# Optimization experiments

Hardware: AMD Instinct MI355X
Metric: run time of the kernel (lower is better)

Reference implementation:

```python
import jax, jax.numpy as jnp
import numpy as np
from jax import lax

EPS = 1e-10

def _ln(x, g, b):
    m = x.mean(-1, keepdims=True)
    v = x.var(-1, keepdims=True)
    return (x - m) / jnp.sqrt(v + 1e-5) * g + b

def _gather(t, idx):
    # t: (B, HW, c), idx: (B, HW, d) -> (B, HW, d, c); out[n,i,k,:] = t[n, idx[n,i,k], :]
    return jax.vmap(lambda tn, In: tn[In])(t, idx)

def setup_inputs() -> dict:
    key = jax.random.key(0)
    ks = jax.random.split(key, 20)
    b, v, c, d, h, w, hid, ksz = 2, 2, 128, 64, 64, 64, 256, 5
    hw = h * w
    Bf = b * v  # v_1 == 1 target view per reference view
    std = 0.02
    return {
        'features_mv': jax.random.normal(ks[0], (b, v, c, h, w), jnp.float32),
        'warp_indices': jax.random.randint(ks[1], (Bf, hw, d), 0, hw, jnp.int32),
        'depth_prob': jax.random.uniform(ks[2], (Bf, hw, d), jnp.float32),
        'ln1_g': jnp.ones((c,), jnp.float32), 'ln1_b': jnp.zeros((c,), jnp.float32),
        'wq': jax.random.normal(ks[3], (c, c), jnp.float32) * std, 'bq': jnp.zeros((c,), jnp.float32),
        'wk': jax.random.normal(ks[4], (c, c), jnp.float32) * std, 'bk': jnp.zeros((c,), jnp.float32),
        'wv': jax.random.normal(ks[5], (c, c), jnp.float32) * std, 'bv': jnp.zeros((c,), jnp.float32),
        'k_pe': jax.random.normal(ks[6], (1, 1, d), jnp.float32) * std,
        'v_pe': jax.random.normal(ks[7], (1, 1, d), jnp.float32) * std,
        'rpe': jax.random.normal(ks[8], (1, 1, d), jnp.float32) * std,
        'proj_w': jax.random.normal(ks[9], (c, c), jnp.float32) * std, 'proj_b': jnp.zeros((c,), jnp.float32),
        'ln2_g': jnp.ones((c,), jnp.float32), 'ln2_b': jnp.zeros((c,), jnp.float32),
        'fc1_w': jax.random.normal(ks[10], (c, hid), jnp.float32) * std, 'fc1_b': jnp.zeros((hid,), jnp.float32),
        'dw_w': jax.random.normal(ks[11], (hid, 1, ksz, ksz), jnp.float32) * std, 'dw_b': jnp.zeros((hid,), jnp.float32),
        'fc2_w': jax.random.normal(ks[12], (hid, c), jnp.float32) * std, 'fc2_b': jnp.zeros((c,), jnp.float32),
    }

def reference(features_mv, warp_indices, depth_prob, ln1_g, ln1_b, wq, bq, wk, bk, wv, bv,
              k_pe, v_pe, rpe, proj_w, proj_b, ln2_g, ln2_b, fc1_w, fc1_b, dw_w, dw_b, fc2_w, fc2_b):
    b, v, c, h, w = features_mv.shape
    hw = h * w
    hid = fc1_w.shape[1]
    scale = c ** (-0.5)  # num_heads = 1 -> head_dim = dim

    # (b v) (h w) c
    x = features_mv.reshape(b * v, c, hw).transpose(0, 2, 1)
    shortcut = x
    xn = _ln(x, ln1_g, ln1_b)
    q = xn @ wq + bq
    k = xn @ wk + bk
    vv = xn @ wv + bv

    # nn pairing: v=2, v_1=1 -> each reference view attends the other view
    Q = (q.reshape(b, v, hw, c) * scale).reshape(b * v, hw, c)
    K = k.reshape(b, v, hw, c)[:, ::-1].reshape(b * v, hw, c)
    V = vv.reshape(b, v, hw, c)[:, ::-1].reshape(b * v, hw, c)

    # SMM_QmK: cost[n,i,k] = sum_c Q[n,i,c] * K[n, idx[n,i,k], c]
    Kg = _gather(K, warp_indices)                       # (B, hw, d, c)
    cost = jnp.einsum('bic,bikc->bik', Q, Kg)
    Q_pe = Q.sum(-1, keepdims=True)                     # (B, hw, 1)
    cost = cost + Q_pe * k_pe + rpe                     # broadcast (1,1,d)

    # (Sim_UNet similarity refinement omitted: UNetModel source unavailable; identity here)
    attn = jax.nn.softmax(cost, axis=-1)
    attn = attn * depth_prob
    attn = (attn + EPS) / (attn.sum(-1, keepdims=True) + EPS)

    # SMM_AmV: out[n,i,c] = sum_k attn[n,i,k] * V[n, idx[n,i,k], c]
    Vg = _gather(V, warp_indices)                       # (B, hw, d, c)
    out = jnp.einsum('bik,bikc->bic', attn, Vg)
    out = out + (attn * v_pe).sum(-1, keepdims=True)

    # projection + residual (v_1 == 1 so B == b*v)
    x = shortcut + (out @ proj_w + proj_b)

    # ConvFFN residual branch
    xn2 = _ln(x, ln2_g, ln2_b)
    y = jax.nn.gelu(xn2 @ fc1_w + fc1_b, approximate=False)
    yi = y.transpose(0, 2, 1).reshape(b * v, hid, h, w)
    yc = lax.conv_general_dilated(yi, dw_w, (1, 1), 'SAME', feature_group_count=hid,
                                  dimension_numbers=('NCHW', 'OIHW', 'NCHW'))
    yc = jax.nn.gelu(yc + dw_b[None, :, None, None], approximate=False)
    y = y + yc.reshape(b * v, hid, hw).transpose(0, 2, 1)
    y = y @ fc2_w + fc2_b
    return x + y
```

## Files before the change

### kernel.cpp

```cpp
#include <hip/hip_runtime.h>
#include <math.h>

#define TOK   16384
#define HW    4096
#define C     128
#define D     64
#define HID   256

constexpr float LN_EPS = 1e-5f;
constexpr float EPS_R  = 1e-10f;
constexpr float QSCALE = 0.08838834764831845f;

typedef __attribute__((ext_vector_type(8))) short  bf16x8;
typedef __attribute__((ext_vector_type(4))) float  f32x4;
#define MFMA16(a, b, c) __builtin_amdgcn_mfma_f32_16x16x32_bf16((a), (b), (c), 0, 0, 0)

__device__ __forceinline__ float bflo(unsigned u) { return __uint_as_float(u << 16); }
__device__ __forceinline__ float bfhi(unsigned u) { return __uint_as_float(u & 0xffff0000u); }
__device__ __forceinline__ float bfu(unsigned short u) { return __uint_as_float((unsigned)u << 16); }
__device__ __forceinline__ unsigned short f2bf(float f) {
  unsigned u = __float_as_uint(f);
  unsigned r = (u + 0x7fffu + ((u >> 16) & 1u)) >> 16;
  return (unsigned short)r;
}
__device__ __forceinline__ float gelu_exact(float x) {
  return 0.5f * x * (1.0f + erff(x * 0.7071067811865476f));
}

__global__ __launch_bounds__(256) void k_prep(const float* __restrict__ wq,
    const float* __restrict__ wk, const float* __restrict__ wv,
    const float* __restrict__ pw, const float* __restrict__ f1w,
    const float* __restrict__ f2w, unsigned short* __restrict__ wt) {
  int id = blockIdx.x * 256 + threadIdx.x;
  if (id < 16384) {
    int n = id >> 7, k = id & 127;
    wt[id] = f2bf(wq[k * 128 + n]);
  } else if (id < 32768) {
    int e = id - 16384; int n = e >> 7, k = e & 127;
    wt[id] = f2bf(wk[k * 128 + n]);
  } else if (id < 49152) {
    int e = id - 32768; int n = e >> 7, k = e & 127;
    wt[id] = f2bf(wv[k * 128 + n]);
  } else if (id < 65536) {
    int e = id - 49152; int n = e >> 7, k = e & 127;
    wt[id] = f2bf(pw[k * 128 + n]);
  } else if (id < 98304) {
    int e = id - 65536; int n = e >> 7, k = e & 127;
    wt[id] = f2bf(f1w[k * 256 + n]);
  } else if (id < 131072) {
    int e = id - 98304; int n = e >> 8, k = e & 255;
    wt[id] = f2bf(f2w[k * 128 + n]);
  }
}

__global__ __launch_bounds__(256) void k_ln1(const float* __restrict__ feat,
    const float* __restrict__ g, const float* __restrict__ b,
    unsigned short* __restrict__ xnb, float* __restrict__ xtm) {
  __shared__ float tile[64][C + 1];
  int t0 = blockIdx.x * 64;
  int n = t0 / HW, i0 = t0 % HW;
  int tid = threadIdx.x;
  const float* fb = feat + (size_t)n * C * HW;
  for (int e = tid; e < 64 * C; e += 256) {
    int ch = e >> 6, ii = e & 63;
    tile[ii][ch] = fb[(size_t)ch * HW + i0 + ii];
  }
  __syncthreads();
  int wave = tid >> 6, lane = tid & 63;
  for (int tkn = wave; tkn < 64; tkn += 4) {
    float a0 = tile[tkn][lane];
    float a1 = tile[tkn][lane + 64];
    float s = a0 + a1;
    for (int off = 32; off; off >>= 1) s += __shfl_xor(s, off, 64);
    float mean = s * (1.0f / 128.0f);
    float d0 = a0 - mean, d1 = a1 - mean;
    float v = d0 * d0 + d1 * d1;
    for (int off = 32; off; off >>= 1) v += __shfl_xor(v, off, 64);
    float rstd = rsqrtf(v * (1.0f / 128.0f) + LN_EPS);
    size_t ro = (size_t)(t0 + tkn) * C;
    xnb[ro + lane]      = f2bf(d0 * rstd * g[lane] + b[lane]);
    xnb[ro + lane + 64] = f2bf(d1 * rstd * g[lane + 64] + b[lane + 64]);
    xtm[ro + lane]      = a0;
    xtm[ro + lane + 64] = a1;
  }
}

__global__ __launch_bounds__(256) void k_qkv(const unsigned short* __restrict__ xnb,
    const unsigned short* __restrict__ wt,
    const float* __restrict__ bq, const float* __restrict__ bk,
    const float* __restrict__ bv, float* __restrict__ q,
    unsigned short* __restrict__ ksw, unsigned short* __restrict__ vsw) {
  int w = threadIdx.x >> 6, lane = threadIdx.x & 63;
  int q4 = lane >> 4, m = lane & 15;
  int t0 = blockIdx.x * 64 + w * 16;
  int wsel = blockIdx.y;
  const unsigned short* Wt = wt + wsel * 16384;
  const unsigned short* ap = xnb + (size_t)(t0 + m) * C + q4 * 8;
  bf16x8 a[4];
  #pragma unroll
  for (int ks = 0; ks < 4; ks++) a[ks] = *(const bf16x8*)(ap + ks * 32);
  f32x4 acc[8];
  #pragma unroll
  for (int nt = 0; nt < 8; nt++) acc[nt] = (f32x4){0.f, 0.f, 0.f, 0.f};
  #pragma unroll
  for (int nt = 0; nt < 8; nt++) {
    const unsigned short* bp = Wt + (size_t)(nt * 16 + m) * C + q4 * 8;
    #pragma unroll
    for (int ks = 0; ks < 4; ks++) {
      bf16x8 bfrag = *(const bf16x8*)(bp + ks * 32);
      acc[nt] = MFMA16(a[ks], bfrag, acc[nt]);
    }
  }
  if (wsel == 0) {
    #pragma unroll
    for (int nt = 0; nt < 8; nt++) {
      int col = nt * 16 + m;
      float bb = bq[col];
      #pragma unroll
      for (int reg = 0; reg < 4; reg++) {
        int row = t0 + q4 * 4 + reg;
        q[(size_t)row * C + col] = (acc[nt][reg] + bb) * QSCALE;
      }
    }
  } else {
    const float* B = (wsel == 1) ? bk : bv;
    unsigned short* O = (wsel == 1) ? ksw : vsw;
    int n = t0 >> 12, i0 = t0 & 4095;
    int tsw = ((n ^ 1) << 12) + i0;
    #pragma unroll
    for (int nt = 0; nt < 8; nt++) {
      int col = nt * 16 + m;
      float bb = B[col];
      #pragma unroll
      for (int reg = 0; reg < 4; reg++) {
        int row = tsw + q4 * 4 + reg;
        O[(size_t)row * C + col] = f2bf(acc[nt][reg] + bb);
      }
    }
  }
}

__global__ __launch_bounds__(256) void k_attn(const float* __restrict__ q,
    const unsigned short* __restrict__ ksw, const unsigned short* __restrict__ vsw,
    const int* __restrict__ widx, const float* __restrict__ dprob,
    const float* __restrict__ kpe, const float* __restrict__ vpe,
    const float* __restrict__ rpe, unsigned short* __restrict__ aoutb) {
  int lane = threadIdx.x & 63;
  int wave = threadIdx.x >> 6;
  int bid = blockIdx.x;
  int n = (bid >> 1) & 3;
  int within = ((bid >> 3) << 1) | (bid & 1);
  int token = n * HW + within * 4 + wave;
  const unsigned short* Kb = ksw + (size_t)n * HW * C;
  const unsigned short* Vb = vsw + (size_t)n * HW * C;
  int g = lane >> 3, s = lane & 7;
  int myidx = widx[token * D + lane];
  float mydp = dprob[token * D + lane];
  float qreg[16];
  const float* qp = q + (size_t)token * C + s * 16;
  #pragma unroll
  for (int i = 0; i < 4; i++) {
    float4 t = *(const float4*)(qp + i * 4);
    qreg[i * 4 + 0] = t.x; qreg[i * 4 + 1] = t.y;
    qreg[i * 4 + 2] = t.z; qreg[i * 4 + 3] = t.w;
  }
  float qpe = 0.f;
  #pragma unroll
  for (int i = 0; i < 16; i++) qpe += qreg[i];
  qpe += __shfl_xor(qpe, 1, 64);
  qpe += __shfl_xor(qpe, 2, 64);
  qpe += __shfl_xor(qpe, 4, 64);
  int rowv[8];
  #pragma unroll
  for (int pass = 0; pass < 8; ++pass)
    rowv[pass] = __shfl(myidx, pass * 8 + g, 64);
  uint4 ka[8], kb[8];
  #pragma unroll
  for (int pass = 0; pass < 8; ++pass) {
    const unsigned short* kr = Kb + (size_t)rowv[pass] * C + s * 16;
    ka[pass] = *(const uint4*)(kr);
    kb[pass] = *(const uint4*)(kr + 8);
  }
  float mycost = 0.f;
  #pragma unroll
  for (int pass = 0; pass < 8; ++pass) {
    float p;
    p  = bflo(ka[pass].x) * qreg[0]  + bfhi(ka[pass].x) * qreg[1];
    p += bflo(ka[pass].y) * qreg[2]  + bfhi(ka[pass].y) * qreg[3];
    p += bflo(ka[pass].z) * qreg[4]  + bfhi(ka[pass].z) * qreg[5];
    p += bflo(ka[pass].w) * qreg[6]  + bfhi(ka[pass].w) * qreg[7];
    p += bflo(kb[pass].x) * qreg[8]  + bfhi(kb[pass].x) * qreg[9];
    p += bflo(kb[pass].y) * qreg[10] + bfhi(kb[pass].y) * qreg[11];
    p += bflo(kb[pass].z) * qreg[12] + bfhi(kb[pass].z) * qreg[13];
    p += bflo(kb[pass].w) * qreg[14] + bfhi(kb[pass].w) * qreg[15];
    p += __shfl_xor(p, 1, 64);
    p += __shfl_xor(p, 2, 64);
    p += __shfl_xor(p, 4, 64);
    float t = __shfl(p, (lane & 7) << 3, 64);
    if (pass == g) mycost = t;
  }
  mycost += qpe * kpe[lane] + rpe[lane];
  float mx = mycost;
  for (int off = 32; off; off >>= 1) mx = fmaxf(mx, __shfl_xor(mx, off, 64));
  float e = __expf(mycost - mx);
  float ssum = e;
  for (int off = 32; off; off >>= 1) ssum += __shfl_xor(ssum, off, 64);
  float attn = (e / ssum) * mydp;
  float s2 = attn;
  for (int off = 32; off; off >>= 1) s2 += __shfl_xor(s2, off, 64);
  attn = (attn + EPS_R) / (s2 + EPS_R);
  float vpt = attn * vpe[lane];
  for (int off = 32; off; off >>= 1) vpt += __shfl_xor(vpt, off, 64);
  float o0 = vpt, o1 = vpt;
  unsigned att_u = __float_as_uint(attn);
  #pragma unroll
  for (int blk = 0; blk < 8; ++blk) {
    unsigned vv[8];
    #pragma unroll
    for (int j = 0; j < 8; j++) {
      int row = __builtin_amdgcn_readlane(myidx, blk * 8 + j);
      vv[j] = *(const unsigned*)(Vb + (size_t)row * C + lane * 2);
    }
    #pragma unroll
    for (int j = 0; j < 8; j++) {
      float a = __uint_as_float(__builtin_amdgcn_readlane(att_u, blk * 8 + j));
      o0 += a * bflo(vv[j]);
      o1 += a * bfhi(vv[j]);
    }
  }
  unsigned pk = (unsigned)f2bf(o0) | ((unsigned)f2bf(o1) << 16);
  *(unsigned*)(aoutb + (size_t)token * C + lane * 2) = pk;
}

__global__ __launch_bounds__(256) void k_projln(const unsigned short* __restrict__ aoutb,
    const unsigned short* __restrict__ wt, const float* __restrict__ pb,
    float* __restrict__ xio, const float* __restrict__ g2,
    const float* __restrict__ b2, unsigned short* __restrict__ xn2b) {
  int w = threadIdx.x >> 6, lane = threadIdx.x & 63;
  int q4 = lane >> 4, m = lane & 15;
  int t0 = blockIdx.x * 64 + w * 16;
  const unsigned short* Wt = wt + 3 * 16384;
  const unsigned short* ap = aoutb + (size_t)(t0 + m) * C + q4 * 8;
  bf16x8 a[4];
  #pragma unroll
  for (int ks = 0; ks < 4; ks++) a[ks] = *(const bf16x8*)(ap + ks * 32);
  f32x4 acc[8];
  #pragma unroll
  for (int nt = 0; nt < 8; nt++) acc[nt] = (f32x4){0.f, 0.f, 0.f, 0.f};
  #pragma unroll
  for (int nt = 0; nt < 8; nt++) {
    const unsigned short* bp = Wt + (size_t)(nt * 16 + m) * C + q4 * 8;
    #pragma unroll
    for (int ks = 0; ks < 4; ks++) {
      bf16x8 bfrag = *(const bf16x8*)(bp + ks * 32);
      acc[nt] = MFMA16(a[ks], bfrag, acc[nt]);
    }
  }
  float s1[4] = {0.f, 0.f, 0.f, 0.f}, s2[4] = {0.f, 0.f, 0.f, 0.f};
  #pragma unroll
  for (int nt = 0; nt < 8; nt++) {
    int col = nt * 16 + m;
    float bb = pb[col];
    #pragma unroll
    for (int reg = 0; reg < 4; reg++) {
      int row = t0 + q4 * 4 + reg;
      float v = acc[nt][reg] + bb + xio[(size_t)row * C + col];
      acc[nt][reg] = v;
      s1[reg] += v;
      s2[reg] += v * v;
    }
  }
  #pragma unroll
  for (int reg = 0; reg < 4; reg++) {
    #pragma unroll
    for (int off = 1; off < 16; off <<= 1) {
      s1[reg] += __shfl_xor(s1[reg], off, 64);
      s2[reg] += __shfl_xor(s2[reg], off, 64);
    }
  }
  float mean[4], rstd[4];
  #pragma unroll
  for (int reg = 0; reg < 4; reg++) {
    mean[reg] = s1[reg] * (1.0f / 128.0f);
    float var = s2[reg] * (1.0f / 128.0f) - mean[reg] * mean[reg];
    rstd[reg] = rsqrtf(var + LN_EPS);
  }
  #pragma unroll
  for (int nt = 0; nt < 8; nt++) {
    int col = nt * 16 + m;
    float gc = g2[col], bc = b2[col];
    #pragma unroll
    for (int reg = 0; reg < 4; reg++) {
      int row = t0 + q4 * 4 + reg;
      float v = acc[nt][reg];
      xio[(size_t)row * C + col] = v;
      xn2b[(size_t)row * C + col] = f2bf((v - mean[reg]) * rstd[reg] * gc + bc);
    }
  }
}

__global__ __launch_bounds__(256) void k_fc1(const unsigned short* __restrict__ xn2b,
    const unsigned short* __restrict__ wt, const float* __restrict__ f1b,
    unsigned short* __restrict__ y) {
  int w = threadIdx.x >> 6, lane = threadIdx.x & 63;
  int q4 = lane >> 4, m = lane & 15;
  int t0 = blockIdx.x * 64 + w * 16;
  int n0 = blockIdx.y * 128;
  const unsigned short* Wt = wt + 65536 + (size_t)n0 * C;
  const unsigned short* ap = xn2b + (size_t)(t0 + m) * C + q4 * 8;
  bf16x8 a[4];
  #pragma unroll
  for (int ks = 0; ks < 4; ks++) a[ks] = *(const bf16x8*)(ap + ks * 32);
  f32x4 acc[8];
  #pragma unroll
  for (int nt = 0; nt < 8; nt++) acc[nt] = (f32x4){0.f, 0.f, 0.f, 0.f};
  #pragma unroll
  for (int nt = 0; nt < 8; nt++) {
    const unsigned short* bp = Wt + (size_t)(nt * 16 + m) * C + q4 * 8;
    #pragma unroll
    for (int ks = 0; ks < 4; ks++) {
      bf16x8 bfrag = *(const bf16x8*)(bp + ks * 32);
      acc[nt] = MFMA16(a[ks], bfrag, acc[nt]);
    }
  }
  #pragma unroll
  for (int nt = 0; nt < 8; nt++) {
    int col = n0 + nt * 16 + m;
    float bb = f1b[col];
    #pragma unroll
    for (int reg = 0; reg < 4; reg++) {
      int row = t0 + q4 * 4 + reg;
      y[(size_t)row * HID + col] = f2bf(gelu_exact(acc[nt][reg] + bb));
    }
  }
}

__global__ __launch_bounds__(256) void k_dwconv(const unsigned short* __restrict__ y,
    const float* __restrict__ w, const float* __restrict__ bias,
    unsigned short* __restrict__ yc) {
  __shared__ float tile[8][401];
  __shared__ float wl[8][25];
  __shared__ float bl[8];
  int bid = blockIdx.x;
  int tile_id = bid & 15;
  int cb = (bid >> 4) & 31;
  int n = bid >> 9;
  int ty = (tile_id >> 2) * 16, tx = (tile_id & 3) * 16;
  int ch0 = cb * 8;
  int tid = threadIdx.x;
  if (tid < 200) wl[tid / 25][tid % 25] = w[(size_t)(ch0 + tid / 25) * 25 + tid % 25];
  if (tid < 8) bl[tid] = bias[ch0 + tid];
  const unsigned short* yb = y + (size_t)n * HW * HID;
  for (int e = tid; e < 400 * 8; e += 256) {
    int cc = e & 7;
    int p = e >> 3;
    int py = p / 20, px = p % 20;
    int gy = ty + py - 2, gx = tx + px - 2;
    float v = 0.f;
    if (gy >= 0 && gy < 64 && gx >= 0 && gx < 64)
      v = bfu(yb[(size_t)(gy * 64 + gx) * HID + ch0 + cc]);
    tile[cc][p] = v;
  }
  __syncthreads();
  int cc = tid & 7;
  int xx = (tid >> 3) & 15;
  int yg = tid >> 7;
  float wreg[25];
  #pragma unroll
  for (int k = 0; k < 25; k++) wreg[k] = wl[cc][k];
  float bb = bl[cc];
  for (int j = 0; j < 8; ++j) {
    int yy = yg * 8 + j;
    float acc = 0.f;
    #pragma unroll
    for (int dy = 0; dy < 5; ++dy)
      #pragma unroll
      for (int dx = 0; dx < 5; ++dx)
        acc += wreg[dy * 5 + dx] * tile[cc][(yy + dy) * 20 + (xx + dx)];
    acc = gelu_exact(acc + bb);
    yc[(size_t)(n * HW + (ty + yy) * 64 + tx + xx) * HID + ch0 + cc] = f2bf(acc);
  }
}

__global__ __launch_bounds__(256) void k_fc2(const unsigned short* __restrict__ y,
    const unsigned short* __restrict__ ycg, const unsigned short* __restrict__ wt,
    const float* __restrict__ f2b, const float* __restrict__ xio,
    float* __restrict__ outp) {
  int w = threadIdx.x >> 6, lane = threadIdx.x & 63;
  int q4 = lane >> 4, m = lane & 15;
  int t0 = blockIdx.x * 64 + w * 16;
  const unsigned short* Wt = wt + 98304;
  const unsigned short* ap = y + (size_t)(t0 + m) * HID + q4 * 8;
  const unsigned short* cp = ycg + (size_t)(t0 + m) * HID + q4 * 8;
  union U { bf16x8 v; unsigned short s[8]; };
  bf16x8 a[8];
  #pragma unroll
  for (int ks = 0; ks < 8; ks++) {
    U ua, uc, ur;
    ua.v = *(const bf16x8*)(ap + ks * 32);
    uc.v = *(const bf16x8*)(cp + ks * 32);
    #pragma unroll
    for (int j = 0; j < 8; j++) ur.s[j] = f2bf(bfu(ua.s[j]) + bfu(uc.s[j]));
    a[ks] = ur.v;
  }
  f32x4 acc[8];
  #pragma unroll
  for (int nt = 0; nt < 8; nt++) acc[nt] = (f32x4){0.f, 0.f, 0.f, 0.f};
  #pragma unroll
  for (int nt = 0; nt < 8; nt++) {
    const unsigned short* bp = Wt + (size_t)(nt * 16 + m) * HID + q4 * 8;
    #pragma unroll
    for (int ks = 0; ks < 8; ks++) {
      bf16x8 bfrag = *(const bf16x8*)(bp + ks * 32);
      acc[nt] = MFMA16(a[ks], bfrag, acc[nt]);
    }
  }
  #pragma unroll
  for (int nt = 0; nt < 8; nt++) {
    int col = nt * 16 + m;
    float bb = f2b[col];
    #pragma unroll
    for (int reg = 0; reg < 4; reg++) {
      int row = t0 + q4 * 4 + reg;
      outp[(size_t)row * C + col] = acc[nt][reg] + bb + xio[(size_t)row * C + col];
    }
  }
}

extern "C" void kernel_launch(void* const* d_in, const int* in_sizes, int n_in,
                              void* d_out, int out_size, void* d_ws, size_t ws_size,
                              hipStream_t stream) {
  (void)in_sizes; (void)n_in; (void)out_size; (void)ws_size;
  const float* feat  = (const float*)d_in[0];
  const int*   widx  = (const int*)d_in[1];
  const float* dprob = (const float*)d_in[2];
  const float* ln1g  = (const float*)d_in[3];
  const float* ln1b  = (const float*)d_in[4];
  const float* wq    = (const float*)d_in[5];
  const float* bq    = (const float*)d_in[6];
  const float* wk    = (const float*)d_in[7];
  const float* bk    = (const float*)d_in[8];
  const float* wv    = (const float*)d_in[9];
  const float* bv    = (const float*)d_in[10];
  const float* kpe   = (const float*)d_in[11];
  const float* vpe   = (const float*)d_in[12];
  const float* rpe   = (const float*)d_in[13];
  const float* pw    = (const float*)d_in[14];
  const float* pb    = (const float*)d_in[15];
  const float* ln2g  = (const float*)d_in[16];
  const float* ln2b  = (const float*)d_in[17];
  const float* f1w   = (const float*)d_in[18];
  const float* f1b   = (const float*)d_in[19];
  const float* dww   = (const float*)d_in[20];
  const float* dwb   = (const float*)d_in[21];
  const float* f2w   = (const float*)d_in[22];
  const float* f2b   = (const float*)d_in[23];

  float* ws = (float*)d_ws;
  const size_t M2 = (size_t)TOK * C;
  float* qb  = ws;
  float* xio = ws + M2;
  unsigned short* xnb   = (unsigned short*)(ws + 2 * M2);
  unsigned short* ksb   = (unsigned short*)(ws + 2 * M2 + M2 / 2);
  unsigned short* vsb   = (unsigned short*)(ws + 3 * M2);
  unsigned short* aoutb = (unsigned short*)(ws + 3 * M2 + M2 / 2);
  unsigned short* xn2b  = (unsigned short*)(ws + 4 * M2);
  unsigned short* yb    = (unsigned short*)(ws + 4 * M2 + M2 / 2);
  unsigned short* ycgb  = (unsigned short*)(ws + 5 * M2 + M2 / 2);
  unsigned short* wtb   = (unsigned short*)(ws + 6 * M2 + M2 / 2);

  k_prep  <<<512, 256, 0, stream>>>(wq, wk, wv, pw, f1w, f2w, wtb);
  k_ln1   <<<TOK / 64, 256, 0, stream>>>(feat, ln1g, ln1b, xnb, xio);
  k_qkv   <<<dim3(TOK / 64, 3), 256, 0, stream>>>(xnb, wtb, bq, bk, bv, qb, ksb, vsb);
  k_attn  <<<TOK / 4, 256, 0, stream>>>(qb, ksb, vsb, widx, dprob, kpe, vpe, rpe, aoutb);
  k_projln<<<TOK / 64, 256, 0, stream>>>(aoutb, wtb, pb, xio, ln2g, ln2b, xn2b);
  k_fc1   <<<dim3(TOK / 64, 2), 256, 0, stream>>>(xn2b, wtb, f1b, yb);
  k_dwconv<<<2048, 256, 0, stream>>>(yb, dww, dwb, ycgb);
  k_fc2   <<<TOK / 64, 256, 0, stream>>>(yb, ycgb, wtb, f2b, xio, (float*)d_out);
}
```

Baseline: 217.3 us.

## Store Q in bf16, read residual from input, register-window dwconv, split fc2

Q is now written and read as bf16 rather than fp32, which halves that buffer's traffic and costs some precision in the attention scores. LN1 no longer writes a token-major fp32 copy of the input. Instead, the projection kernel reads the residual directly from the channel-major feature tensor, trading a write plus a read for strided reads. The depthwise conv preloads a 12x5 window into registers so rows are reused across its 8 outputs. fc2 is split into two column halves across blockIdx.y to double the grid.

```diff
diff --git a/kernel.cpp b/kernel.cpp
--- a/kernel.cpp
+++ b/kernel.cpp
@@ -55,7 +55,7 @@
 
 __global__ __launch_bounds__(256) void k_ln1(const float* __restrict__ feat,
     const float* __restrict__ g, const float* __restrict__ b,
-    unsigned short* __restrict__ xnb, float* __restrict__ xtm) {
+    unsigned short* __restrict__ xnb) {
   __shared__ float tile[64][C + 1];
   int t0 = blockIdx.x * 64;
   int n = t0 / HW, i0 = t0 % HW;
@@ -80,15 +80,13 @@
     size_t ro = (size_t)(t0 + tkn) * C;
     xnb[ro + lane]      = f2bf(d0 * rstd * g[lane] + b[lane]);
     xnb[ro + lane + 64] = f2bf(d1 * rstd * g[lane + 64] + b[lane + 64]);
-    xtm[ro + lane]      = a0;
-    xtm[ro + lane + 64] = a1;
   }
 }
 
 __global__ __launch_bounds__(256) void k_qkv(const unsigned short* __restrict__ xnb,
     const unsigned short* __restrict__ wt,
     const float* __restrict__ bq, const float* __restrict__ bk,
-    const float* __restrict__ bv, float* __restrict__ q,
+    const float* __restrict__ bv, unsigned short* __restrict__ qb,
     unsigned short* __restrict__ ksw, unsigned short* __restrict__ vsw) {
   int w = threadIdx.x >> 6, lane = threadIdx.x & 63;
   int q4 = lane >> 4, m = lane & 15;
@@ -111,36 +109,24 @@
       acc[nt] = MFMA16(a[ks], bfrag, acc[nt]);
     }
   }
-  if (wsel == 0) {
-    #pragma unroll
-    for (int nt = 0; nt < 8; nt++) {
-      int col = nt * 16 + m;
-      float bb = bq[col];
-      #pragma unroll
-      for (int reg = 0; reg < 4; reg++) {
-        int row = t0 + q4 * 4 + reg;
-        q[(size_t)row * C + col] = (acc[nt][reg] + bb) * QSCALE;
-      }
-    }
-  } else {
-    const float* B = (wsel == 1) ? bk : bv;
-    unsigned short* O = (wsel == 1) ? ksw : vsw;
-    int n = t0 >> 12, i0 = t0 & 4095;
-    int tsw = ((n ^ 1) << 12) + i0;
-    #pragma unroll
-    for (int nt = 0; nt < 8; nt++) {
-      int col = nt * 16 + m;
-      float bb = B[col];
-      #pragma unroll
-      for (int reg = 0; reg < 4; reg++) {
-        int row = tsw + q4 * 4 + reg;
-        O[(size_t)row * C + col] = f2bf(acc[nt][reg] + bb);
-      }
-    }
-  }
-}
-
-__global__ __launch_bounds__(256) void k_attn(const float* __restrict__ q,
+  const float* B = (wsel == 0) ? bq : ((wsel == 1) ? bk : bv);
+  float sc = (wsel == 0) ? QSCALE : 1.0f;
+  unsigned short* O = (wsel == 0) ? qb : ((wsel == 1) ? ksw : vsw);
+  int n = t0 >> 12, i0 = t0 & 4095;
+  int base = (wsel == 0) ? t0 : (((n ^ 1) << 12) + i0);
+  #pragma unroll
+  for (int nt = 0; nt < 8; nt++) {
+    int col = nt * 16 + m;
+    float bb = B[col];
+    #pragma unroll
+    for (int reg = 0; reg < 4; reg++) {
+      int row = base + q4 * 4 + reg;
+      O[(size_t)row * C + col] = f2bf((acc[nt][reg] + bb) * sc);
+    }
+  }
+}
+
+__global__ __launch_bounds__(256) void k_attn(const unsigned short* __restrict__ qb,
     const unsigned short* __restrict__ ksw, const unsigned short* __restrict__ vsw,
     const int* __restrict__ widx, const float* __restrict__ dprob,
     const float* __restrict__ kpe, const float* __restrict__ vpe,
@@ -157,12 +143,18 @@
   int myidx = widx[token * D + lane];
   float mydp = dprob[token * D + lane];
   float qreg[16];
-  const float* qp = q + (size_t)token * C + s * 16;
-  #pragma unroll
-  for (int i = 0; i < 4; i++) {
-    float4 t = *(const float4*)(qp + i * 4);
-    qreg[i * 4 + 0] = t.x; qreg[i * 4 + 1] = t.y;
-    qreg[i * 4 + 2] = t.z; qreg[i * 4 + 3] = t.w;
+  {
+    const unsigned short* qp = qb + (size_t)token * C + s * 16;
+    uint4 qa = *(const uint4*)(qp);
+    uint4 qbv = *(const uint4*)(qp + 8);
+    qreg[0] = bflo(qa.x);  qreg[1] = bfhi(qa.x);
+    qreg[2] = bflo(qa.y);  qreg[3] = bfhi(qa.y);
+    qreg[4] = bflo(qa.z);  qreg[5] = bfhi(qa.z);
+    qreg[6] = bflo(qa.w);  qreg[7] = bfhi(qa.w);
+    qreg[8] = bflo(qbv.x); qreg[9] = bfhi(qbv.x);
+    qreg[10] = bflo(qbv.y); qreg[11] = bfhi(qbv.y);
+    qreg[12] = bflo(qbv.z); qreg[13] = bfhi(qbv.z);
+    qreg[14] = bflo(qbv.w); qreg[15] = bfhi(qbv.w);
   }
   float qpe = 0.f;
   #pragma unroll
@@ -234,8 +226,9 @@
 
 __global__ __launch_bounds__(256) void k_projln(const unsigned short* __restrict__ aoutb,
     const unsigned short* __restrict__ wt, const float* __restrict__ pb,
-    float* __restrict__ xio, const float* __restrict__ g2,
-    const float* __restrict__ b2, unsigned short* __restrict__ xn2b) {
+    const float* __restrict__ feat, float* __restrict__ xio,
+    const float* __restrict__ g2, const float* __restrict__ b2,
+    unsigned short* __restrict__ xn2b) {
   int w = threadIdx.x >> 6, lane = threadIdx.x & 63;
   int q4 = lane >> 4, m = lane & 15;
   int t0 = blockIdx.x * 64 + w * 16;
@@ -256,15 +249,16 @@
       acc[nt] = MFMA16(a[ks], bfrag, acc[nt]);
     }
   }
+  int nview = t0 >> 12, ibase = (t0 & 4095) + q4 * 4;
   float s1[4] = {0.f, 0.f, 0.f, 0.f}, s2[4] = {0.f, 0.f, 0.f, 0.f};
   #pragma unroll
   for (int nt = 0; nt < 8; nt++) {
     int col = nt * 16 + m;
     float bb = pb[col];
+    const float* fp = feat + ((size_t)nview * C + col) * HW + ibase;
     #pragma unroll
     for (int reg = 0; reg < 4; reg++) {
-      int row = t0 + q4 * 4 + reg;
-      float v = acc[nt][reg] + bb + xio[(size_t)row * C + col];
+      float v = acc[nt][reg] + bb + fp[reg];
       acc[nt][reg] = v;
       s1[reg] += v;
       s2[reg] += v * v;
@@ -369,15 +363,22 @@
   #pragma unroll
   for (int k = 0; k < 25; k++) wreg[k] = wl[cc][k];
   float bb = bl[cc];
+  float win[12][5];
+  #pragma unroll
+  for (int r = 0; r < 12; r++)
+    #pragma unroll
+    for (int dx = 0; dx < 5; dx++)
+      win[r][dx] = tile[cc][(yg * 8 + r) * 20 + xx + dx];
+  #pragma unroll
   for (int j = 0; j < 8; ++j) {
-    int yy = yg * 8 + j;
     float acc = 0.f;
     #pragma unroll
     for (int dy = 0; dy < 5; ++dy)
       #pragma unroll
       for (int dx = 0; dx < 5; ++dx)
-        acc += wreg[dy * 5 + dx] * tile[cc][(yy + dy) * 20 + (xx + dx)];
+        acc += wreg[dy * 5 + dx] * win[j + dy][dx];
     acc = gelu_exact(acc + bb);
+    int yy = yg * 8 + j;
     yc[(size_t)(n * HW + (ty + yy) * 64 + tx + xx) * HID + ch0 + cc] = f2bf(acc);
   }
 }
@@ -389,6 +390,7 @@
   int w = threadIdx.x >> 6, lane = threadIdx.x & 63;
   int q4 = lane >> 4, m = lane & 15;
   int t0 = blockIdx.x * 64 + w * 16;
+  int half = blockIdx.y;
   const unsigned short* Wt = wt + 98304;
   const unsigned short* ap = y + (size_t)(t0 + m) * HID + q4 * 8;
   const unsigned short* cp = ycg + (size_t)(t0 + m) * HID + q4 * 8;
@@ -403,12 +405,12 @@
     for (int j = 0; j < 8; j++) ur.s[j] = f2bf(bfu(ua.s[j]) + bfu(uc.s[j]));
     a[ks] = ur.v;
   }
-  f32x4 acc[8];
-  #pragma unroll
-  for (int nt = 0; nt < 8; nt++) acc[nt] = (f32x4){0.f, 0.f, 0.f, 0.f};
-  #pragma unroll
-  for (int nt = 0; nt < 8; nt++) {
-    const unsigned short* bp = Wt + (size_t)(nt * 16 + m) * HID + q4 * 8;
+  f32x4 acc[4];
+  #pragma unroll
+  for (int nt = 0; nt < 4; nt++) acc[nt] = (f32x4){0.f, 0.f, 0.f, 0.f};
+  #pragma unroll
+  for (int nt = 0; nt < 4; nt++) {
+    const unsigned short* bp = Wt + (size_t)(half * 64 + nt * 16 + m) * HID + q4 * 8;
     #pragma unroll
     for (int ks = 0; ks < 8; ks++) {
       bf16x8 bfrag = *(const bf16x8*)(bp + ks * 32);
@@ -416,8 +418,8 @@
     }
   }
   #pragma unroll
-  for (int nt = 0; nt < 8; nt++) {
-    int col = nt * 16 + m;
+  for (int nt = 0; nt < 4; nt++) {
+    int col = half * 64 + nt * 16 + m;
     float bb = f2b[col];
     #pragma unroll
     for (int reg = 0; reg < 4; reg++) {
@@ -458,23 +460,23 @@
 
   float* ws = (float*)d_ws;
   const size_t M2 = (size_t)TOK * C;
-  float* qb  = ws;
-  float* xio = ws + M2;
-  unsigned short* xnb   = (unsigned short*)(ws + 2 * M2);
-  unsigned short* ksb   = (unsigned short*)(ws + 2 * M2 + M2 / 2);
-  unsigned short* vsb   = (unsigned short*)(ws + 3 * M2);
-  unsigned short* aoutb = (unsigned short*)(ws + 3 * M2 + M2 / 2);
-  unsigned short* xn2b  = (unsigned short*)(ws + 4 * M2);
-  unsigned short* yb    = (unsigned short*)(ws + 4 * M2 + M2 / 2);
-  unsigned short* ycgb  = (unsigned short*)(ws + 5 * M2 + M2 / 2);
-  unsigned short* wtb   = (unsigned short*)(ws + 6 * M2 + M2 / 2);
+  float* xio = ws;
+  unsigned short* qbb   = (unsigned short*)(ws + M2);
+  unsigned short* xnb   = (unsigned short*)(ws + M2 + M2 / 2);
+  unsigned short* ksb   = (unsigned short*)(ws + 2 * M2);
+  unsigned short* vsb   = (unsigned short*)(ws + 2 * M2 + M2 / 2);
+  unsigned short* aoutb = (unsigned short*)(ws + 3 * M2);
+  unsigned short* xn2b  = (unsigned short*)(ws + 3 * M2 + M2 / 2);
+  unsigned short* yb    = (unsigned short*)(ws + 4 * M2);
+  unsigned short* ycgb  = (unsigned short*)(ws + 5 * M2);
+  unsigned short* wtb   = (unsigned short*)(ws + 6 * M2);
 
   k_prep  <<<512, 256, 0, stream>>>(wq, wk, wv, pw, f1w, f2w, wtb);
-  k_ln1   <<<TOK / 64, 256, 0, stream>>>(feat, ln1g, ln1b, xnb, xio);
-  k_qkv   <<<dim3(TOK / 64, 3), 256, 0, stream>>>(xnb, wtb, bq, bk, bv, qb, ksb, vsb);
-  k_attn  <<<TOK / 4, 256, 0, stream>>>(qb, ksb, vsb, widx, dprob, kpe, vpe, rpe, aoutb);
-  k_projln<<<TOK / 64, 256, 0, stream>>>(aoutb, wtb, pb, xio, ln2g, ln2b, xn2b);
+  k_ln1   <<<TOK / 64, 256, 0, stream>>>(feat, ln1g, ln1b, xnb);
+  k_qkv   <<<dim3(TOK / 64, 3), 256, 0, stream>>>(xnb, wtb, bq, bk, bv, qbb, ksb, vsb);
+  k_attn  <<<TOK / 4, 256, 0, stream>>>(qbb, ksb, vsb, widx, dprob, kpe, vpe, rpe, aoutb);
+  k_projln<<<TOK / 64, 256, 0, stream>>>(aoutb, wtb, pb, feat, xio, ln2g, ln2b, xn2b);
   k_fc1   <<<dim3(TOK / 64, 2), 256, 0, stream>>>(xn2b, wtb, f1b, yb);
   k_dwconv<<<2048, 256, 0, stream>>>(yb, dww, dwb, ycgb);
-  k_fc2   <<<TOK / 64, 256, 0, stream>>>(yb, ycgb, wtb, f2b, xio, (float*)d_out);
-}
+  k_fc2   <<<dim3(TOK / 64, 2), 256, 0, stream>>>(yb, ycgb, wtb, f2b, xio, (float*)d_out);
+}
```

After: 216.5 us. No clear change (-0.4%).
